# Performance work log

Hardware: AMD Instinct MI355X
Metric: run time of the kernel (lower is better)

The kernel has to match this reference:

```python
import jax, jax.numpy as jnp
import numpy as np

B, T, C, H = 4, 2048, 1024, 16
NEG = -1e9  # masked-fill value (finite to keep grads clean)


def setup_inputs() -> dict:
    key = jax.random.key(0)
    ks = jax.random.split(key, 5)
    s = 1.0 / np.sqrt(C)  # keep logits O(1) like trained linear layers
    return {
        "x": jax.random.normal(ks[0], (B, T, C), dtype=jnp.float32),
        "wq": jax.random.normal(ks[1], (C, C), dtype=jnp.float32) * s,
        "bq": jnp.zeros((C,), dtype=jnp.float32),
        "wk": jax.random.normal(ks[2], (C, C), dtype=jnp.float32) * s,
        "bk": jnp.zeros((C,), dtype=jnp.float32),
        "wv": jax.random.normal(ks[3], (C, C), dtype=jnp.float32) * s,
        "bv": jnp.zeros((C,), dtype=jnp.float32),
        "wo": jax.random.normal(ks[4], (C, C), dtype=jnp.float32) * s,
        "bo": jnp.zeros((C,), dtype=jnp.float32),
    }


def _split_heads(y):
    # [B,T,C] -> [B,H,T,hd]
    b, t, c = y.shape
    return y.reshape(b, t, H, c // H).transpose(0, 2, 1, 3)


def reference(x, wq, bq, wk, bk, wv, bv, wo, bo):
    b, t, c = x.shape
    scale = (c // H) ** (-0.5)
    q = _split_heads(x @ wq.T + bq)  # [B,H,T,hd]
    k = _split_heads(x @ wk.T + bk)
    v = _split_heads(x @ wv.T + bv)
    att = jnp.einsum("bhqd,bhkd->bhqk", q, k) * scale  # [B,H,T,T]
    causal = jnp.tril(jnp.ones((t, t), dtype=bool))
    att = jnp.where(causal[None, None], att, NEG)
    att = jax.nn.softmax(att, axis=-1)  # dropout is identity in eval mode
    y = jnp.einsum("bhqk,bhkd->bhqd", att, v)
    y = y.transpose(0, 2, 1, 3).reshape(b, t, c)
    return y @ wo.T + bo
```

## Files before the change

### kernel.cpp

```cpp
#include <hip/hip_runtime.h>


#define B_ 4
#define T_ 2048
#define C_ 1024
#define H_ 16
#define M_ 8192

typedef unsigned short u16;
typedef __bf16 bf16x8 __attribute__((ext_vector_type(8)));
typedef float f32x4 __attribute__((ext_vector_type(4)));

static __device__ __forceinline__ u16 f2bf(float f) {
  unsigned int u = __float_as_uint(f);
  u += 0x7fffu + ((u >> 16) & 1u);
  return (u16)(u >> 16);
}

static __device__ __forceinline__ void async16(const void* g, void* l) {
  __builtin_amdgcn_global_load_lds(
      (const __attribute__((address_space(1))) unsigned int*)g,
      (__attribute__((address_space(3))) unsigned int*)l, 16, 0, 0);
}

#if __has_builtin(__builtin_amdgcn_exp2f)
#define EXP2F(x) __builtin_amdgcn_exp2f(x)
#else
#define EXP2F(x) exp2f(x)
#endif

static __device__ __forceinline__ f32x4 mfma32(bf16x8 a, bf16x8 b, f32x4 c) {
  return __builtin_amdgcn_mfma_f32_16x16x32_bf16(a, b, c, 0, 0, 0);
}

static __device__ __forceinline__ unsigned int cvtpk(float lo, float hi) {
  unsigned int r;
  asm("v_cvt_pk_bf16_f32 %0, %1, %2" : "=v"(r) : "v"(lo), "v"(hi));
  return r;
}

#define FENCE() asm volatile("" ::: "memory")

__global__ __launch_bounds__(256) void cvt_all(const float* __restrict__ x,
                                               const float* __restrict__ w0,
                                               const float* __restrict__ w1,
                                               const float* __restrict__ w2,
                                               const float* __restrict__ w3,
                                               u16* __restrict__ xb,
                                               u16* __restrict__ wb,
                                               float s0) {
  const int NX = M_ * C_ / 4, NW = C_ * C_ / 4;
  int i = blockIdx.x * 256 + threadIdx.x;
  const float* src;
  u16* dst;
  int idx;
  float s = 1.f;
  if (i < NX) {
    src = x; dst = xb; idx = i;
  } else {
    int j = i - NX;
    int w = j / NW;
    idx = j - w * NW;
    src = (w == 0) ? w0 : (w == 1) ? w1 : (w == 2) ? w2 : w3;
    dst = wb + (size_t)w * C_ * C_;
    if (w == 0) s = s0;
  }
  float4 f = ((const float4*)src)[idx];
  ushort4 o;
  o.x = f2bf(f.x * s); o.y = f2bf(f.y * s); o.z = f2bf(f.z * s); o.w = f2bf(f.w * s);
  ((ushort4*)dst)[idx] = o;
}

__global__ __launch_bounds__(512, 1) void gemm_qkv(const u16* __restrict__ A,
                                                   const u16* __restrict__ W,
                                                   const float* __restrict__ bq,
                                                   const float* __restrict__ bk,
                                                   const float* __restrict__ bv,
                                                   float qscale,
                                                   u16* __restrict__ outqk,
                                                   u16* __restrict__ vtb) {
  __shared__ __align__(16) union {
    u16 buf[3][24576];
    u16 Cu[256 * 136];
    u16 Ct[128 * 272];
  } sm;
  const int tid = threadIdx.x, lane = tid & 63, wave = tid >> 6;
  const int quad = lane >> 4, l16 = lane & 15;
  const int wm = wave >> 1, wn = wave & 1;
  const int bid = blockIdx.x;
  const int xcd = bid & 7, idx = bid >> 3;
  const int cq = idx >> 2;
  const int row0 = (xcd * 4 + (idx & 3)) * 256;
  const int sel = cq >> 3, colw = cq & 7;
  const int col0 = colw * 128;
  const u16* Bt = W + (size_t)sel * C_ * C_;
  const float* bias = sel == 0 ? bq : (sel == 1 ? bk : bv);
  const float bscale = sel == 0 ? qscale : 1.f;

  const u16* aptr[4];
  const u16* bptr[2];
#pragma unroll
  for (int it = 0; it < 4; it++) {
    int c = it * 512 + tid, r = c >> 3, g = (c & 7) ^ (r & 7);
    aptr[it] = A + (size_t)(row0 + r) * C_ + g * 8;
  }
#pragma unroll
  for (int it = 0; it < 2; it++) {
    int c = it * 512 + tid, r = c >> 3, g = (c & 7) ^ (r & 7);
    bptr[it] = Bt + (size_t)(col0 + r) * C_ + g * 8;
  }

  auto STAGE = [&](int t, int pp) {
    const int k0 = t * 64;
    u16* lA = sm.buf[pp];
    u16* lB = sm.buf[pp] + 16384;
#pragma unroll
    for (int it = 0; it < 4; it++)
      async16(aptr[it] + k0, lA + (size_t)(it * 512 + wave * 64) * 8);
#pragma unroll
    for (int it = 0; it < 2; it++)
      async16(bptr[it] + k0, lB + (size_t)(it * 512 + wave * 64) * 8);
  };

  f32x4 zero = {0.f, 0.f, 0.f, 0.f};
  f32x4 acc[4][4];
#pragma unroll
  for (int i = 0; i < 4; i++)
#pragma unroll
    for (int j = 0; j < 4; j++) acc[i][j] = zero;

  STAGE(0, 0);
  STAGE(1, 1);

  int p = 0, p2 = 2;
#pragma unroll 1
  for (int u = 0; u < 16; ++u) {
    FENCE();
    __builtin_amdgcn_s_barrier();
    FENCE();
    if (u < 14) STAGE(u + 2, p2);
    if (u < 14) {
      asm volatile("s_waitcnt vmcnt(12)" ::: "memory");
    } else if (u < 15) {
      asm volatile("s_waitcnt vmcnt(6)" ::: "memory");
    } else {
      asm volatile("s_waitcnt vmcnt(0)" ::: "memory");
    }
    FENCE();
    __builtin_amdgcn_s_barrier();
    FENCE();

    const u16* As = sm.buf[p];
    const u16* Bs = sm.buf[p] + 16384;
    bf16x8 bfr[4][2];
#pragma unroll
    for (int j = 0; j < 4; j++) {
      int rn = wn * 64 + 16 * j + l16;
#pragma unroll
      for (int kk = 0; kk < 2; kk++)
        bfr[j][kk] =
            *(const bf16x8*)(Bs + rn * 64 + (((kk * 4 + quad) ^ (rn & 7)) * 8));
    }
    {
      bf16x8 a2[2][2];
#pragma unroll
      for (int i = 0; i < 2; i++) {
        int rm = wm * 64 + 16 * i + l16;
#pragma unroll
        for (int kk = 0; kk < 2; kk++)
          a2[i][kk] =
              *(const bf16x8*)(As + rm * 64 + (((kk * 4 + quad) ^ (rm & 7)) * 8));
      }
      __builtin_amdgcn_s_setprio(1);
#pragma unroll
      for (int i = 0; i < 2; i++)
#pragma unroll
        for (int j = 0; j < 4; j++) {
          acc[i][j] = mfma32(a2[i][0], bfr[j][0], acc[i][j]);
          acc[i][j] = mfma32(a2[i][1], bfr[j][1], acc[i][j]);
        }
      __builtin_amdgcn_s_setprio(0);
    }
    FENCE();
    __builtin_amdgcn_s_barrier();
    FENCE();
    {
      bf16x8 a2[2][2];
#pragma unroll
      for (int i = 0; i < 2; i++) {
        int rm = wm * 64 + 16 * (i + 2) + l16;
#pragma unroll
        for (int kk = 0; kk < 2; kk++)
          a2[i][kk] =
              *(const bf16x8*)(As + rm * 64 + (((kk * 4 + quad) ^ (rm & 7)) * 8));
      }
      __builtin_amdgcn_s_setprio(1);
#pragma unroll
      for (int i = 0; i < 2; i++)
#pragma unroll
        for (int j = 0; j < 4; j++) {
          acc[i + 2][j] = mfma32(a2[i][0], bfr[j][0], acc[i + 2][j]);
          acc[i + 2][j] = mfma32(a2[i][1], bfr[j][1], acc[i + 2][j]);
        }
      __builtin_amdgcn_s_setprio(0);
    }
    asm volatile("s_waitcnt lgkmcnt(0)" ::: "memory");
    p = (p == 2) ? 0 : p + 1;
    p2 = (p2 == 2) ? 0 : p2 + 1;
  }
  __syncthreads();

  float bj[4];
#pragma unroll
  for (int j = 0; j < 4; j++) bj[j] = bias[col0 + wn * 64 + 16 * j + l16] * bscale;

  if (sel == 2) {
#pragma unroll
    for (int i = 0; i < 4; i++)
#pragma unroll
      for (int j = 0; j < 4; j++) {
        int lc = wn * 64 + 16 * j + l16;
        int rt = wm * 64 + 16 * i + quad * 4;
        union { u16 s[4]; uint2 u; } w;
#pragma unroll
        for (int r = 0; r < 4; r++) w.s[r] = f2bf(acc[i][j][r] + bj[j]);
        *(uint2*)(sm.Ct + (size_t)lc * 272 + rt) = w.u;
      }
    __syncthreads();
    const int bb = row0 >> 11, t0 = row0 & 2047;
#pragma unroll
    for (int c2 = 0; c2 < 8; c2++) {
      int c = c2 * 512 + tid;
      int nr = c >> 5, ch = c & 31;
      bf16x8 v = *(const bf16x8*)(sm.Ct + (size_t)nr * 272 + ch * 8);
      int gn = col0 + nr, d = gn & 63, hh = gn >> 6;
      *(bf16x8*)(vtb + ((size_t)((bb * 16 + hh) * 64 + d)) * T_ + t0 + ch * 8) = v;
    }
  } else {
#pragma unroll
    for (int i = 0; i < 4; i++)
#pragma unroll
      for (int j = 0; j < 4; j++) {
        int lc = wn * 64 + 16 * j + l16;
        int rt = wm * 64 + 16 * i + quad * 4;
#pragma unroll
        for (int r = 0; r < 4; r++)
          sm.Cu[(size_t)(rt + r) * 136 + lc] = f2bf(acc[i][j][r] + bj[j]);
      }
    __syncthreads();
    u16* dst = outqk + (size_t)sel * M_ * C_;
#pragma unroll
    for (int c2 = 0; c2 < 8; c2++) {
      int c = c2 * 512 + tid;
      int rw = c >> 4, ch = c & 15;
      bf16x8 v = *(const bf16x8*)(sm.Cu + (size_t)rw * 136 + ch * 8);
      *(bf16x8*)(dst + (size_t)(row0 + rw) * C_ + col0 + ch * 8) = v;
    }
  }
}

__global__ __launch_bounds__(512, 1) void gemm_o(const u16* __restrict__ A,
                                                 const u16* __restrict__ Bt,
                                                 const float* __restrict__ bias,
                                                 float* __restrict__ outf) {
  __shared__ __align__(16) union {
    u16 buf[3][24576];
    float Cf[256 * 132];
  } sm;
  const int tid = threadIdx.x, lane = tid & 63, wave = tid >> 6;
  const int quad = lane >> 4, l16 = lane & 15;
  const int wm = wave >> 1, wn = wave & 1;
  const int bid = blockIdx.x;
  const int xcd = bid & 7, idx = bid >> 3;
  const int row0 = (xcd * 4 + (idx & 3)) * 256;
  const int col0 = (idx >> 2) * 128;

  const u16* aptr[4];
  const u16* bptr[2];
#pragma unroll
  for (int it = 0; it < 4; it++) {
    int c = it * 512 + tid, r = c >> 3, g = (c & 7) ^ (r & 7);
    aptr[it] = A + (size_t)(row0 + r) * C_ + g * 8;
  }
#pragma unroll
  for (int it = 0; it < 2; it++) {
    int c = it * 512 + tid, r = c >> 3, g = (c & 7) ^ (r & 7);
    bptr[it] = Bt + (size_t)(col0 + r) * C_ + g * 8;
  }

  auto STAGE = [&](int t, int pp) {
    const int k0 = t * 64;
    u16* lA = sm.buf[pp];
    u16* lB = sm.buf[pp] + 16384;
#pragma unroll
    for (int it = 0; it < 4; it++)
      async16(aptr[it] + k0, lA + (size_t)(it * 512 + wave * 64) * 8);
#pragma unroll
    for (int it = 0; it < 2; it++)
      async16(bptr[it] + k0, lB + (size_t)(it * 512 + wave * 64) * 8);
  };

  f32x4 zero = {0.f, 0.f, 0.f, 0.f};
  f32x4 acc[4][4];
#pragma unroll
  for (int i = 0; i < 4; i++)
#pragma unroll
    for (int j = 0; j < 4; j++) acc[i][j] = zero;

  STAGE(0, 0);
  STAGE(1, 1);

  int p = 0, p2 = 2;
#pragma unroll 1
  for (int u = 0; u < 16; ++u) {
    FENCE();
    __builtin_amdgcn_s_barrier();
    FENCE();
    if (u < 14) STAGE(u + 2, p2);
    if (u < 14) {
      asm volatile("s_waitcnt vmcnt(12)" ::: "memory");
    } else if (u < 15) {
      asm volatile("s_waitcnt vmcnt(6)" ::: "memory");
    } else {
      asm volatile("s_waitcnt vmcnt(0)" ::: "memory");
    }
    FENCE();
    __builtin_amdgcn_s_barrier();
    FENCE();

    const u16* As = sm.buf[p];
    const u16* Bs = sm.buf[p] + 16384;
    bf16x8 bfr[4][2];
#pragma unroll
    for (int j = 0; j < 4; j++) {
      int rn = wn * 64 + 16 * j + l16;
#pragma unroll
      for (int kk = 0; kk < 2; kk++)
        bfr[j][kk] =
            *(const bf16x8*)(Bs + rn * 64 + (((kk * 4 + quad) ^ (rn & 7)) * 8));
    }
    {
      bf16x8 a2[2][2];
#pragma unroll
      for (int i = 0; i < 2; i++) {
        int rm = wm * 64 + 16 * i + l16;
#pragma unroll
        for (int kk = 0; kk < 2; kk++)
          a2[i][kk] =
              *(const bf16x8*)(As + rm * 64 + (((kk * 4 + quad) ^ (rm & 7)) * 8));
      }
      __builtin_amdgcn_s_setprio(1);
#pragma unroll
      for (int i = 0; i < 2; i++)
#pragma unroll
        for (int j = 0; j < 4; j++) {
          acc[i][j] = mfma32(a2[i][0], bfr[j][0], acc[i][j]);
          acc[i][j] = mfma32(a2[i][1], bfr[j][1], acc[i][j]);
        }
      __builtin_amdgcn_s_setprio(0);
    }
    FENCE();
    __builtin_amdgcn_s_barrier();
    FENCE();
    {
      bf16x8 a2[2][2];
#pragma unroll
      for (int i = 0; i < 2; i++) {
        int rm = wm * 64 + 16 * (i + 2) + l16;
#pragma unroll
        for (int kk = 0; kk < 2; kk++)
          a2[i][kk] =
              *(const bf16x8*)(As + rm * 64 + (((kk * 4 + quad) ^ (rm & 7)) * 8));
      }
      __builtin_amdgcn_s_setprio(1);
#pragma unroll
      for (int i = 0; i < 2; i++)
#pragma unroll
        for (int j = 0; j < 4; j++) {
          acc[i + 2][j] = mfma32(a2[i][0], bfr[j][0], acc[i + 2][j]);
          acc[i + 2][j] = mfma32(a2[i][1], bfr[j][1], acc[i + 2][j]);
        }
      __builtin_amdgcn_s_setprio(0);
    }
    asm volatile("s_waitcnt lgkmcnt(0)" ::: "memory");
    p = (p == 2) ? 0 : p + 1;
    p2 = (p2 == 2) ? 0 : p2 + 1;
  }
  __syncthreads();

  float bj[4];
#pragma unroll
  for (int j = 0; j < 4; j++) bj[j] = bias[col0 + wn * 64 + 16 * j + l16];

#pragma unroll
  for (int i = 0; i < 4; i++)
#pragma unroll
    for (int j = 0; j < 4; j++) {
      int lc = wn * 64 + 16 * j + l16;
      int rt = wm * 64 + 16 * i + quad * 4;
#pragma unroll
      for (int r = 0; r < 4; r++)
        sm.Cf[(size_t)(rt + r) * 132 + lc] = acc[i][j][r] + bj[j];
    }
  __syncthreads();
#pragma unroll
  for (int c2 = 0; c2 < 16; c2++) {
    int c = c2 * 512 + tid;
    int rw = c >> 5, c4 = c & 31;
    float4 v = *(const float4*)(sm.Cf + (size_t)rw * 132 + c4 * 4);
    *(float4*)(outf + (size_t)(row0 + rw) * C_ + col0 + c4 * 4) = v;
  }
}

__global__ __launch_bounds__(256) void attn(const u16* __restrict__ q,
                                            const u16* __restrict__ k,
                                            const u16* __restrict__ vt,
                                            u16* __restrict__ y) {
  __shared__ __align__(16) u16 Ksm[128 * 64];
  __shared__ __align__(16) u16 Vsm[2][64 * 64];
  const int tid = threadIdx.x, lane = tid & 63, wave = tid >> 6;
  const int quad = lane >> 4, l16 = lane & 15;
  static const int qperm[16] = {15, 14, 11, 10, 12, 13, 8, 9, 3, 2, 7, 6, 0, 1, 4, 5};
  const int bh = blockIdx.x;
  const int qt = qperm[blockIdx.y];
  const int b = bh >> 4, h = bh & 15;

  const int S0 = ((lane & 15) + ((lane >> 4) & 1) * 32) * 4;
  const int S1 = S0 + 64;
  const bool hi32 = (lane & 32) != 0;

  bf16x8 qf[2][2];
#pragma unroll
  for (int m = 0; m < 2; m++) {
    const u16* qp =
        q + (size_t)(b * T_ + qt * 128 + wave * 32 + m * 16 + l16) * C_ + h * 64;
#pragma unroll
    for (int ks = 0; ks < 2; ks++)
      qf[m][ks] = *(const bf16x8*)(qp + ks * 32 + quad * 8);
  }

  f32x4 zero = {0.f, 0.f, 0.f, 0.f};
  f32x4 o[2][4];
  float lps[2] = {0.f, 0.f};
#pragma unroll
  for (int m = 0; m < 2; m++)
#pragma unroll
    for (int dt = 0; dt < 4; dt++) o[m][dt] = zero;

  const u16* kp[4];
  const u16* vp[4];
#pragma unroll
  for (int i = 0; i < 4; i++) {
    int c = i * 256 + tid;
    int r = c >> 3, lc = (c & 7) ^ (r & 7);
    kp[i] = k + (size_t)(b * T_ + r) * C_ + h * 64 + lc * 8;
  }
#pragma unroll
  for (int s = 0; s < 2; s++)
#pragma unroll
    for (int i = 0; i < 2; i++) {
      int c = i * 256 + tid;
      int r = c >> 3, lc = (c & 7) ^ (r & 7);
      vp[s * 2 + i] = vt + (size_t)(bh * 64 + r) * T_ + 64 * s + lc * 8;
    }

  const int qrow = wave * 32 + l16;

#pragma unroll 1
  for (int jt = 0; jt <= qt; ++jt) {
#pragma unroll
    for (int i = 0; i < 4; i++) {
      async16(kp[i], Ksm + (size_t)(i * 256 + wave * 64) * 8);
      kp[i] += (size_t)128 * C_;
    }
#pragma unroll
    for (int s = 0; s < 2; s++)
#pragma unroll
      for (int i = 0; i < 2; i++) {
        async16(vp[s * 2 + i], Vsm[s] + (size_t)(i * 256 + wave * 64) * 8);
        vp[s * 2 + i] += 128;
      }
    __syncthreads();

    const bool diag = (jt == qt);
#pragma unroll
    for (int hh = 0; hh < 2; ++hh) {
      if (diag && (2 * wave + 2 - 4 * hh) <= 0) continue;
      unsigned int pk[2][4][2];
#pragma unroll
      for (int n = 0; n < 4; ++n) {
        int rk = hh * 64 + n * 16 + l16;
        bf16x8 kf0 = *(const bf16x8*)(Ksm + rk * 64 + ((quad ^ (rk & 7)) * 8));
        bf16x8 kf1 = *(const bf16x8*)(Ksm + rk * 64 + (((4 + quad) ^ (rk & 7)) * 8));
#pragma unroll
        for (int m = 0; m < 2; ++m) {
          int nlim = diag ? (2 * wave + m + 1 - 4 * hh) : 4;
          float e[4];
          if (n < nlim) {
            f32x4 s = mfma32(kf0, qf[m][0], zero);
            s = mfma32(kf1, qf[m][1], s);
#pragma unroll
            for (int r = 0; r < 4; r++) e[r] = EXP2F(s[r]);
            if (diag) {
              int rmax = qrow + m * 16 - hh * 64 - n * 16 - quad * 4;
#pragma unroll
              for (int r = 0; r < 4; r++)
                if (r > rmax) e[r] = 0.f;
            }
            lps[m] += (e[0] + e[1]) + (e[2] + e[3]);
          } else {
#pragma unroll
            for (int r = 0; r < 4; r++) e[r] = 0.f;
          }
          pk[m][n][0] = cvtpk(e[0], e[1]);
          pk[m][n][1] = cvtpk(e[2], e[3]);
        }
      }
      bf16x8 pa[2][2];
#pragma unroll
      for (int m = 0; m < 2; ++m)
#pragma unroll
        for (int ks = 0; ks < 2; ++ks) {
          union { unsigned int u[4]; bf16x8 v; } uu;
#pragma unroll
          for (int c = 0; c < 2; ++c) {
            int x = (int)pk[m][2 * ks][c];
            int yv = (int)pk[m][2 * ks + 1][c];
            int bx0 = __builtin_amdgcn_ds_bpermute(S0, x);
            int by0 = __builtin_amdgcn_ds_bpermute(S0, yv);
            int bx1 = __builtin_amdgcn_ds_bpermute(S1, x);
            int by1 = __builtin_amdgcn_ds_bpermute(S1, yv);
            uu.u[c] = (unsigned int)(hi32 ? by0 : bx0);
            uu.u[2 + c] = (unsigned int)(hi32 ? by1 : bx1);
          }
          pa[m][ks] = uu.v;
        }
#pragma unroll
      for (int dt = 0; dt < 4; ++dt) {
        int rv = dt * 16 + l16;
        bf16x8 vf0 = *(const bf16x8*)(Vsm[hh] + rv * 64 + ((quad ^ (rv & 7)) * 8));
        bf16x8 vf1 = *(const bf16x8*)(Vsm[hh] + rv * 64 + (((4 + quad) ^ (rv & 7)) * 8));
#pragma unroll
        for (int m = 0; m < 2; m++) {
          o[m][dt] = mfma32(pa[m][0], vf0, o[m][dt]);
          o[m][dt] = mfma32(pa[m][1], vf1, o[m][dt]);
        }
      }
    }
    __syncthreads();
  }

  float linv[2];
#pragma unroll
  for (int m = 0; m < 2; m++) {
    float v = lps[m];
    v += __shfl_xor(v, 16);
    v += __shfl_xor(v, 32);
    linv[m] = 1.f / v;
  }

#pragma unroll
  for (int m = 0; m < 2; m++)
#pragma unroll
    for (int r = 0; r < 4; r++) {
      float il = __shfl(linv[m], quad * 4 + r);
      int grow = b * T_ + qt * 128 + wave * 32 + m * 16 + quad * 4 + r;
#pragma unroll
      for (int dt = 0; dt < 4; dt++)
        y[(size_t)grow * C_ + h * 64 + dt * 16 + l16] = f2bf(o[m][dt][r] * il);
    }
}

extern "C" void kernel_launch(void* const* d_in, const int* in_sizes, int n_in,
                              void* d_out, int out_size, void* d_ws, size_t ws_size,
                              hipStream_t stream) {
  const float* x  = (const float*)d_in[0];
  const float* wq = (const float*)d_in[1];
  const float* bq = (const float*)d_in[2];
  const float* wk = (const float*)d_in[3];
  const float* bk = (const float*)d_in[4];
  const float* wv = (const float*)d_in[5];
  const float* bv = (const float*)d_in[6];
  const float* wo = (const float*)d_in[7];
  const float* bo = (const float*)d_in[8];
  float* out = (float*)d_out;

  const float QSCALE = 0.125f * 1.4426950408889634f;

  u16* xb  = (u16*)d_ws;
  u16* wqb = xb  + (size_t)M_ * C_;
  u16* wob = wqb + 3 * (size_t)C_ * C_;
  u16* qb  = wob + (size_t)C_ * C_;
  u16* kb  = qb  + (size_t)M_ * C_;
  u16* vtb = kb  + (size_t)M_ * C_;
  u16* yb  = xb;

  const int NCVT = (M_ * C_ + 4 * C_ * C_) / 4 / 256;
  cvt_all<<<NCVT, 256, 0, stream>>>(x, wq, wk, wv, wo, xb, wqb, QSCALE);

  gemm_qkv<<<768, 512, 0, stream>>>(xb, wqb, bq, bk, bv, QSCALE, qb, vtb);

  attn<<<dim3(B_ * H_, 16), 256, 0, stream>>>(qb, kb, vtb, yb);

  gemm_o<<<256, 512, 0, stream>>>(yb, wob, bo, out);
}
```

Baseline: 251.5 us.

## Enlarge QKV GEMM tile to 256x256 with double-buffered LDS pipeline

Each QKV projection block now computes a 256x256 output tile instead of 256x128, and the grid shrinks from 768 to 384 blocks. Waves are arranged 2x4, and each wave holds 8x4 accumulators. The three-stage LDS ring is replaced by two buffers, with the next stage issued after the compute and its barrier. The aim is to raise arithmetic intensity and cut redundant A-tile loads. In exchange, register pressure rises, there is less latency hiding from the shallower pipeline, and 384 blocks may fill the 256 CUs unevenly.

Measured after the change: 255.0 us. No clear change (+1.4%).

```diff
diff --git a/kernel.cpp b/kernel.cpp
--- a/kernel.cpp
+++ b/kernel.cpp
@@ -80,33 +80,29 @@
                                                    u16* __restrict__ outqk,
                                                    u16* __restrict__ vtb) {
   __shared__ __align__(16) union {
-    u16 buf[3][24576];
-    u16 Cu[256 * 136];
-    u16 Ct[128 * 272];
+    u16 buf[2][32768];
+    u16 Cu[256 * 264];
+    u16 Ct[256 * 272];
   } sm;
   const int tid = threadIdx.x, lane = tid & 63, wave = tid >> 6;
   const int quad = lane >> 4, l16 = lane & 15;
-  const int wm = wave >> 1, wn = wave & 1;
+  const int wm = wave >> 2, wn = wave & 3;
   const int bid = blockIdx.x;
-  const int xcd = bid & 7, idx = bid >> 3;
-  const int cq = idx >> 2;
-  const int row0 = (xcd * 4 + (idx & 3)) * 256;
-  const int sel = cq >> 3, colw = cq & 7;
-  const int col0 = colw * 128;
+  const int xcd = bid & 7, lid = bid >> 3;
+  const int cq = lid >> 2, rloc = lid & 3;
+  const int row0 = (xcd * 4 + rloc) * 256;
+  const int sel = cq >> 2, colw = cq & 3;
+  const int col0 = colw * 256;
   const u16* Bt = W + (size_t)sel * C_ * C_;
   const float* bias = sel == 0 ? bq : (sel == 1 ? bk : bv);
   const float bscale = sel == 0 ? qscale : 1.f;
 
   const u16* aptr[4];
-  const u16* bptr[2];
+  const u16* bptr[4];
 #pragma unroll
   for (int it = 0; it < 4; it++) {
     int c = it * 512 + tid, r = c >> 3, g = (c & 7) ^ (r & 7);
     aptr[it] = A + (size_t)(row0 + r) * C_ + g * 8;
-  }
-#pragma unroll
-  for (int it = 0; it < 2; it++) {
-    int c = it * 512 + tid, r = c >> 3, g = (c & 7) ^ (r & 7);
     bptr[it] = Bt + (size_t)(col0 + r) * C_ + g * 8;
   }
 
@@ -118,31 +114,25 @@
     for (int it = 0; it < 4; it++)
       async16(aptr[it] + k0, lA + (size_t)(it * 512 + wave * 64) * 8);
 #pragma unroll
-    for (int it = 0; it < 2; it++)
+    for (int it = 0; it < 4; it++)
       async16(bptr[it] + k0, lB + (size_t)(it * 512 + wave * 64) * 8);
   };
 
   f32x4 zero = {0.f, 0.f, 0.f, 0.f};
-  f32x4 acc[4][4];
-#pragma unroll
-  for (int i = 0; i < 4; i++)
+  f32x4 acc[8][4];
+#pragma unroll
+  for (int i = 0; i < 8; i++)
 #pragma unroll
     for (int j = 0; j < 4; j++) acc[i][j] = zero;
 
   STAGE(0, 0);
   STAGE(1, 1);
 
-  int p = 0, p2 = 2;
 #pragma unroll 1
   for (int u = 0; u < 16; ++u) {
-    FENCE();
-    __builtin_amdgcn_s_barrier();
-    FENCE();
-    if (u < 14) STAGE(u + 2, p2);
-    if (u < 14) {
-      asm volatile("s_waitcnt vmcnt(12)" ::: "memory");
-    } else if (u < 15) {
-      asm volatile("s_waitcnt vmcnt(6)" ::: "memory");
+    const int cur = u & 1;
+    if (u < 15) {
+      asm volatile("s_waitcnt vmcnt(8)" ::: "memory");
     } else {
       asm volatile("s_waitcnt vmcnt(0)" ::: "memory");
     }
@@ -150,65 +140,40 @@
     __builtin_amdgcn_s_barrier();
     FENCE();
 
-    const u16* As = sm.buf[p];
-    const u16* Bs = sm.buf[p] + 16384;
-    bf16x8 bfr[4][2];
-#pragma unroll
-    for (int j = 0; j < 4; j++) {
-      int rn = wn * 64 + 16 * j + l16;
-#pragma unroll
-      for (int kk = 0; kk < 2; kk++)
-        bfr[j][kk] =
-            *(const bf16x8*)(Bs + rn * 64 + (((kk * 4 + quad) ^ (rn & 7)) * 8));
-    }
-    {
-      bf16x8 a2[2][2];
-#pragma unroll
-      for (int i = 0; i < 2; i++) {
-        int rm = wm * 64 + 16 * i + l16;
-#pragma unroll
-        for (int kk = 0; kk < 2; kk++)
-          a2[i][kk] =
-              *(const bf16x8*)(As + rm * 64 + (((kk * 4 + quad) ^ (rm & 7)) * 8));
+    const u16* As = sm.buf[cur];
+    const u16* Bs = sm.buf[cur] + 16384;
+#pragma unroll
+    for (int kk = 0; kk < 2; kk++) {
+      bf16x8 bv[4], av[8];
+#pragma unroll
+      for (int j = 0; j < 4; j++) {
+        int rn = wn * 64 + 16 * j + l16;
+        bv[j] = *(const bf16x8*)(Bs + rn * 64 + (((kk * 4 + quad) ^ (rn & 7)) * 8));
+      }
+#pragma unroll
+      for (int i = 0; i < 8; i++) {
+        int rm = wm * 128 + 16 * i + l16;
+        av[i] = *(const bf16x8*)(As + rm * 64 + (((kk * 4 + quad) ^ (rm & 7)) * 8));
       }
       __builtin_amdgcn_s_setprio(1);
 #pragma unroll
-      for (int i = 0; i < 2; i++)
-#pragma unroll
-        for (int j = 0; j < 4; j++) {
-          acc[i][j] = mfma32(a2[i][0], bfr[j][0], acc[i][j]);
-          acc[i][j] = mfma32(a2[i][1], bfr[j][1], acc[i][j]);
-        }
+      for (int i = 0; i < 8; i++)
+#pragma unroll
+        for (int j = 0; j < 4; j++)
+          acc[i][j] = mfma32(av[i], bv[j], acc[i][j]);
       __builtin_amdgcn_s_setprio(0);
-    }
+      if (kk == 0) {
+        FENCE();
+        __builtin_amdgcn_s_barrier();
+        FENCE();
+      }
+    }
+    asm volatile("s_waitcnt lgkmcnt(0)" ::: "memory");
     FENCE();
     __builtin_amdgcn_s_barrier();
     FENCE();
-    {
-      bf16x8 a2[2][2];
-#pragma unroll
-      for (int i = 0; i < 2; i++) {
-        int rm = wm * 64 + 16 * (i + 2) + l16;
-#pragma unroll
-        for (int kk = 0; kk < 2; kk++)
-          a2[i][kk] =
-              *(const bf16x8*)(As + rm * 64 + (((kk * 4 + quad) ^ (rm & 7)) * 8));
-      }
-      __builtin_amdgcn_s_setprio(1);
-#pragma unroll
-      for (int i = 0; i < 2; i++)
-#pragma unroll
-        for (int j = 0; j < 4; j++) {
-          acc[i + 2][j] = mfma32(a2[i][0], bfr[j][0], acc[i + 2][j]);
-          acc[i + 2][j] = mfma32(a2[i][1], bfr[j][1], acc[i + 2][j]);
-        }
-      __builtin_amdgcn_s_setprio(0);
-    }
-    asm volatile("s_waitcnt lgkmcnt(0)" ::: "memory");
-    p = (p == 2) ? 0 : p + 1;
-    p2 = (p2 == 2) ? 0 : p2 + 1;
-  }
-  __syncthreads();
+    if (u + 2 < 16) STAGE(u + 2, cur);
+  }
 
   float bj[4];
 #pragma unroll
@@ -216,11 +181,11 @@
 
   if (sel == 2) {
 #pragma unroll
-    for (int i = 0; i < 4; i++)
+    for (int i = 0; i < 8; i++)
 #pragma unroll
       for (int j = 0; j < 4; j++) {
         int lc = wn * 64 + 16 * j + l16;
-        int rt = wm * 64 + 16 * i + quad * 4;
+        int rt = wm * 128 + 16 * i + quad * 4;
         union { u16 s[4]; uint2 u; } w;
 #pragma unroll
         for (int r = 0; r < 4; r++) w.s[r] = f2bf(acc[i][j][r] + bj[j]);
@@ -229,7 +194,7 @@
     __syncthreads();
     const int bb = row0 >> 11, t0 = row0 & 2047;
 #pragma unroll
-    for (int c2 = 0; c2 < 8; c2++) {
+    for (int c2 = 0; c2 < 16; c2++) {
       int c = c2 * 512 + tid;
       int nr = c >> 5, ch = c & 31;
       bf16x8 v = *(const bf16x8*)(sm.Ct + (size_t)nr * 272 + ch * 8);
@@ -238,22 +203,22 @@
     }
   } else {
 #pragma unroll
-    for (int i = 0; i < 4; i++)
+    for (int i = 0; i < 8; i++)
 #pragma unroll
       for (int j = 0; j < 4; j++) {
         int lc = wn * 64 + 16 * j + l16;
-        int rt = wm * 64 + 16 * i + quad * 4;
+        int rt = wm * 128 + 16 * i + quad * 4;
 #pragma unroll
         for (int r = 0; r < 4; r++)
-          sm.Cu[(size_t)(rt + r) * 136 + lc] = f2bf(acc[i][j][r] + bj[j]);
+          sm.Cu[(size_t)(rt + r) * 264 + lc] = f2bf(acc[i][j][r] + bj[j]);
       }
     __syncthreads();
     u16* dst = outqk + (size_t)sel * M_ * C_;
 #pragma unroll
-    for (int c2 = 0; c2 < 8; c2++) {
+    for (int c2 = 0; c2 < 16; c2++) {
       int c = c2 * 512 + tid;
-      int rw = c >> 4, ch = c & 15;
-      bf16x8 v = *(const bf16x8*)(sm.Cu + (size_t)rw * 136 + ch * 8);
+      int rw = c >> 5, ch = c & 31;
+      bf16x8 v = *(const bf16x8*)(sm.Cu + (size_t)rw * 264 + ch * 8);
       *(bf16x8*)(dst + (size_t)(row0 + rw) * C_ + col0 + ch * 8) = v;
     }
   }
@@ -598,7 +563,7 @@
   const int NCVT = (M_ * C_ + 4 * C_ * C_) / 4 / 256;
   cvt_all<<<NCVT, 256, 0, stream>>>(x, wq, wk, wv, wo, xb, wqb, QSCALE);
 
-  gemm_qkv<<<768, 512, 0, stream>>>(xb, wqb, bq, bk, bv, QSCALE, qb, vtb);
+  gemm_qkv<<<384, 512, 0, stream>>>(xb, wqb, bq, bk, bv, QSCALE, qb, vtb);
 
   attn<<<dim3(B_ * H_, 16), 256, 0, stream>>>(qb, kb, vtb, yb);
 
```

## Interleave async global-to-LDS loads across four MFMA sub-phases per k-tile

Applied to the files above, without the earlier changes.

Restructures the main loop of the QKV and output-projection GEMMs. The async global-to-LDS staging of the next tile is now spread across four compute sub-phases split by k-half and row-half, instead of one bulk issue at the top of each iteration. The two barriers per iteration become four smaller phases, each reading LDS fragments, issuing one or two async copies, then running its MFMAs. The aim is to spread memory issue across the compute and shrink the stall at the tile boundary, at the cost of more barriers and lgkmcnt waits per k-tile.

Result: slower. 263.2 us (+4.7%).

```diff
diff --git a/kernel.cpp b/kernel.cpp
--- a/kernel.cpp
+++ b/kernel.cpp
@@ -40,6 +40,7 @@
 }
 
 #define FENCE() asm volatile("" ::: "memory")
+#define LGKM0() asm volatile("s_waitcnt lgkmcnt(0)" ::: "memory")
 
 __global__ __launch_bounds__(256) void cvt_all(const float* __restrict__ x,
                                                const float* __restrict__ w0,
@@ -110,16 +111,12 @@
     bptr[it] = Bt + (size_t)(col0 + r) * C_ + g * 8;
   }
 
-  auto STAGE = [&](int t, int pp) {
-    const int k0 = t * 64;
-    u16* lA = sm.buf[pp];
-    u16* lB = sm.buf[pp] + 16384;
-#pragma unroll
-    for (int it = 0; it < 4; it++)
-      async16(aptr[it] + k0, lA + (size_t)(it * 512 + wave * 64) * 8);
-#pragma unroll
-    for (int it = 0; it < 2; it++)
-      async16(bptr[it] + k0, lB + (size_t)(it * 512 + wave * 64) * 8);
+  auto SA = [&](int t, int pp, int it) {
+    async16(aptr[it] + t * 64, sm.buf[pp] + (size_t)(it * 512 + wave * 64) * 8);
+  };
+  auto SB = [&](int t, int pp, int it) {
+    async16(bptr[it] + t * 64,
+            sm.buf[pp] + 16384 + (size_t)(it * 512 + wave * 64) * 8);
   };
 
   f32x4 zero = {0.f, 0.f, 0.f, 0.f};
@@ -129,84 +126,113 @@
 #pragma unroll
     for (int j = 0; j < 4; j++) acc[i][j] = zero;
 
-  STAGE(0, 0);
-  STAGE(1, 1);
-
-  int p = 0, p2 = 2;
+#pragma unroll
+  for (int it = 0; it < 4; it++) SA(0, 0, it);
+  SB(0, 0, 0); SB(0, 0, 1);
+#pragma unroll
+  for (int it = 0; it < 4; it++) SA(1, 1, it);
+  SB(1, 1, 0); SB(1, 1, 1);
+  asm volatile("s_waitcnt vmcnt(6)" ::: "memory");
+  FENCE();
+  __builtin_amdgcn_s_barrier();
+  FENCE();
+
 #pragma unroll 1
-  for (int u = 0; u < 16; ++u) {
-    FENCE();
-    __builtin_amdgcn_s_barrier();
-    FENCE();
-    if (u < 14) STAGE(u + 2, p2);
-    if (u < 14) {
-      asm volatile("s_waitcnt vmcnt(12)" ::: "memory");
-    } else if (u < 15) {
-      asm volatile("s_waitcnt vmcnt(6)" ::: "memory");
-    } else {
-      asm volatile("s_waitcnt vmcnt(0)" ::: "memory");
-    }
-    FENCE();
-    __builtin_amdgcn_s_barrier();
-    FENCE();
-
-    const u16* As = sm.buf[p];
-    const u16* Bs = sm.buf[p] + 16384;
-    bf16x8 bfr[4][2];
-#pragma unroll
-    for (int j = 0; j < 4; j++) {
-      int rn = wn * 64 + 16 * j + l16;
-#pragma unroll
-      for (int kk = 0; kk < 2; kk++)
-        bfr[j][kk] =
-            *(const bf16x8*)(Bs + rn * 64 + (((kk * 4 + quad) ^ (rn & 7)) * 8));
-    }
-    {
-      bf16x8 a2[2][2];
-#pragma unroll
-      for (int i = 0; i < 2; i++) {
-        int rm = wm * 64 + 16 * i + l16;
-#pragma unroll
-        for (int kk = 0; kk < 2; kk++)
-          a2[i][kk] =
-              *(const bf16x8*)(As + rm * 64 + (((kk * 4 + quad) ^ (rm & 7)) * 8));
-      }
-      __builtin_amdgcn_s_setprio(1);
-#pragma unroll
-      for (int i = 0; i < 2; i++)
-#pragma unroll
-        for (int j = 0; j < 4; j++) {
-          acc[i][j] = mfma32(a2[i][0], bfr[j][0], acc[i][j]);
-          acc[i][j] = mfma32(a2[i][1], bfr[j][1], acc[i][j]);
-        }
-      __builtin_amdgcn_s_setprio(0);
-    }
-    FENCE();
-    __builtin_amdgcn_s_barrier();
-    FENCE();
-    {
-      bf16x8 a2[2][2];
-#pragma unroll
-      for (int i = 0; i < 2; i++) {
-        int rm = wm * 64 + 16 * (i + 2) + l16;
-#pragma unroll
-        for (int kk = 0; kk < 2; kk++)
-          a2[i][kk] =
-              *(const bf16x8*)(As + rm * 64 + (((kk * 4 + quad) ^ (rm & 7)) * 8));
-      }
-      __builtin_amdgcn_s_setprio(1);
-#pragma unroll
-      for (int i = 0; i < 2; i++)
-#pragma unroll
-        for (int j = 0; j < 4; j++) {
-          acc[i + 2][j] = mfma32(a2[i][0], bfr[j][0], acc[i + 2][j]);
-          acc[i + 2][j] = mfma32(a2[i][1], bfr[j][1], acc[i + 2][j]);
-        }
-      __builtin_amdgcn_s_setprio(0);
-    }
-    asm volatile("s_waitcnt lgkmcnt(0)" ::: "memory");
-    p = (p == 2) ? 0 : p + 1;
-    p2 = (p2 == 2) ? 0 : p2 + 1;
+  for (int t = 0; t < 16; ++t) {
+    const int cur = t % 3, dst = (t + 2) % 3;
+    const bool st = (t < 14);
+    const u16* As = sm.buf[cur];
+    const u16* Bs = sm.buf[cur] + 16384;
+
+    bf16x8 av0, av1, bv0[4];
+    {
+      int rm0 = wm * 64 + l16, rm1 = wm * 64 + 16 + l16;
+      av0 = *(const bf16x8*)(As + rm0 * 64 + ((quad ^ (rm0 & 7)) * 8));
+      av1 = *(const bf16x8*)(As + rm1 * 64 + ((quad ^ (rm1 & 7)) * 8));
+#pragma unroll
+      for (int j = 0; j < 4; j++) {
+        int rn = wn * 64 + 16 * j + l16;
+        bv0[j] = *(const bf16x8*)(Bs + rn * 64 + ((quad ^ (rn & 7)) * 8));
+      }
+      if (st) { SA(t + 2, dst, 0); SA(t + 2, dst, 1); }
+      LGKM0();
+      FENCE();
+      __builtin_amdgcn_s_setprio(1);
+#pragma unroll
+      for (int j = 0; j < 4; j++) {
+        acc[0][j] = mfma32(av0, bv0[j], acc[0][j]);
+        acc[1][j] = mfma32(av1, bv0[j], acc[1][j]);
+      }
+      __builtin_amdgcn_s_setprio(0);
+      FENCE();
+      __builtin_amdgcn_s_barrier();
+      FENCE();
+    }
+    {
+      int rm2 = wm * 64 + 32 + l16, rm3 = wm * 64 + 48 + l16;
+      bf16x8 av2 = *(const bf16x8*)(As + rm2 * 64 + ((quad ^ (rm2 & 7)) * 8));
+      bf16x8 av3 = *(const bf16x8*)(As + rm3 * 64 + ((quad ^ (rm3 & 7)) * 8));
+      if (st) { SA(t + 2, dst, 2); SA(t + 2, dst, 3); }
+      LGKM0();
+      FENCE();
+      __builtin_amdgcn_s_setprio(1);
+#pragma unroll
+      for (int j = 0; j < 4; j++) {
+        acc[2][j] = mfma32(av2, bv0[j], acc[2][j]);
+        acc[3][j] = mfma32(av3, bv0[j], acc[3][j]);
+      }
+      __builtin_amdgcn_s_setprio(0);
+      FENCE();
+      __builtin_amdgcn_s_barrier();
+      FENCE();
+    }
+    bf16x8 bv1[4];
+    {
+      int rm0 = wm * 64 + l16, rm1 = wm * 64 + 16 + l16;
+      bf16x8 av0b = *(const bf16x8*)(As + rm0 * 64 + (((4 + quad) ^ (rm0 & 7)) * 8));
+      bf16x8 av1b = *(const bf16x8*)(As + rm1 * 64 + (((4 + quad) ^ (rm1 & 7)) * 8));
+#pragma unroll
+      for (int j = 0; j < 4; j++) {
+        int rn = wn * 64 + 16 * j + l16;
+        bv1[j] = *(const bf16x8*)(Bs + rn * 64 + (((4 + quad) ^ (rn & 7)) * 8));
+      }
+      if (st) SB(t + 2, dst, 0);
+      LGKM0();
+      FENCE();
+      __builtin_amdgcn_s_setprio(1);
+#pragma unroll
+      for (int j = 0; j < 4; j++) {
+        acc[0][j] = mfma32(av0b, bv1[j], acc[0][j]);
+        acc[1][j] = mfma32(av1b, bv1[j], acc[1][j]);
+      }
+      __builtin_amdgcn_s_setprio(0);
+      FENCE();
+      __builtin_amdgcn_s_barrier();
+      FENCE();
+    }
+    {
+      int rm2 = wm * 64 + 32 + l16, rm3 = wm * 64 + 48 + l16;
+      bf16x8 av2b = *(const bf16x8*)(As + rm2 * 64 + (((4 + quad) ^ (rm2 & 7)) * 8));
+      bf16x8 av3b = *(const bf16x8*)(As + rm3 * 64 + (((4 + quad) ^ (rm3 & 7)) * 8));
+      if (st) SB(t + 2, dst, 1);
+      LGKM0();
+      FENCE();
+      __builtin_amdgcn_s_setprio(1);
+#pragma unroll
+      for (int j = 0; j < 4; j++) {
+        acc[2][j] = mfma32(av2b, bv1[j], acc[2][j]);
+        acc[3][j] = mfma32(av3b, bv1[j], acc[3][j]);
+      }
+      __builtin_amdgcn_s_setprio(0);
+      if (t <= 13) {
+        asm volatile("s_waitcnt vmcnt(6)" ::: "memory");
+      } else if (t == 14) {
+        asm volatile("s_waitcnt vmcnt(0)" ::: "memory");
+      }
+      FENCE();
+      __builtin_amdgcn_s_barrier();
+      FENCE();
+    }
   }
   __syncthreads();
 
@@ -248,13 +274,13 @@
           sm.Cu[(size_t)(rt + r) * 136 + lc] = f2bf(acc[i][j][r] + bj[j]);
       }
     __syncthreads();
-    u16* dst = outqk + (size_t)sel * M_ * C_;
+    u16* dst2 = outqk + (size_t)sel * M_ * C_;
 #pragma unroll
     for (int c2 = 0; c2 < 8; c2++) {
       int c = c2 * 512 + tid;
       int rw = c >> 4, ch = c & 15;
       bf16x8 v = *(const bf16x8*)(sm.Cu + (size_t)rw * 136 + ch * 8);
-      *(bf16x8*)(dst + (size_t)(row0 + rw) * C_ + col0 + ch * 8) = v;
+      *(bf16x8*)(dst2 + (size_t)(row0 + rw) * C_ + col0 + ch * 8) = v;
     }
   }
 }
@@ -288,16 +314,12 @@
     bptr[it] = Bt + (size_t)(col0 + r) * C_ + g * 8;
   }
 
-  auto STAGE = [&](int t, int pp) {
-    const int k0 = t * 64;
-    u16* lA = sm.buf[pp];
-    u16* lB = sm.buf[pp] + 16384;
-#pragma unroll
-    for (int it = 0; it < 4; it++)
-      async16(aptr[it] + k0, lA + (size_t)(it * 512 + wave * 64) * 8);
-#pragma unroll
-    for (int it = 0; it < 2; it++)
-      async16(bptr[it] + k0, lB + (size_t)(it * 512 + wave * 64) * 8);
+  auto SA = [&](int t, int pp, int it) {
+    async16(aptr[it] + t * 64, sm.buf[pp] + (size_t)(it * 512 + wave * 64) * 8);
+  };
+  auto SB = [&](int t, int pp, int it) {
+    async16(bptr[it] + t * 64,
+            sm.buf[pp] + 16384 + (size_t)(it * 512 + wave * 64) * 8);
   };
 
   f32x4 zero = {0.f, 0.f, 0.f, 0.f};
@@ -307,84 +329,113 @@
 #pragma unroll
     for (int j = 0; j < 4; j++) acc[i][j] = zero;
 
-  STAGE(0, 0);
-  STAGE(1, 1);
-
-  int p = 0, p2 = 2;
+#pragma unroll
+  for (int it = 0; it < 4; it++) SA(0, 0, it);
+  SB(0, 0, 0); SB(0, 0, 1);
+#pragma unroll
+  for (int it = 0; it < 4; it++) SA(1, 1, it);
+  SB(1, 1, 0); SB(1, 1, 1);
+  asm volatile("s_waitcnt vmcnt(6)" ::: "memory");
+  FENCE();
+  __builtin_amdgcn_s_barrier();
+  FENCE();
+
 #pragma unroll 1
-  for (int u = 0; u < 16; ++u) {
-    FENCE();
-    __builtin_amdgcn_s_barrier();
-    FENCE();
-    if (u < 14) STAGE(u + 2, p2);
-    if (u < 14) {
-      asm volatile("s_waitcnt vmcnt(12)" ::: "memory");
-    } else if (u < 15) {
-      asm volatile("s_waitcnt vmcnt(6)" ::: "memory");
-    } else {
-      asm volatile("s_waitcnt vmcnt(0)" ::: "memory");
-    }
-    FENCE();
-    __builtin_amdgcn_s_barrier();
-    FENCE();
-
-    const u16* As = sm.buf[p];
-    const u16* Bs = sm.buf[p] + 16384;
-    bf16x8 bfr[4][2];
-#pragma unroll
-    for (int j = 0; j < 4; j++) {
-      int rn = wn * 64 + 16 * j + l16;
-#pragma unroll
-      for (int kk = 0; kk < 2; kk++)
-        bfr[j][kk] =
-            *(const bf16x8*)(Bs + rn * 64 + (((kk * 4 + quad) ^ (rn & 7)) * 8));
-    }
-    {
-      bf16x8 a2[2][2];
-#pragma unroll
-      for (int i = 0; i < 2; i++) {
-        int rm = wm * 64 + 16 * i + l16;
-#pragma unroll
-        for (int kk = 0; kk < 2; kk++)
-          a2[i][kk] =
-              *(const bf16x8*)(As + rm * 64 + (((kk * 4 + quad) ^ (rm & 7)) * 8));
-      }
-      __builtin_amdgcn_s_setprio(1);
-#pragma unroll
-      for (int i = 0; i < 2; i++)
-#pragma unroll
-        for (int j = 0; j < 4; j++) {
-          acc[i][j] = mfma32(a2[i][0], bfr[j][0], acc[i][j]);
-          acc[i][j] = mfma32(a2[i][1], bfr[j][1], acc[i][j]);
-        }
-      __builtin_amdgcn_s_setprio(0);
-    }
-    FENCE();
-    __builtin_amdgcn_s_barrier();
-    FENCE();
-    {
-      bf16x8 a2[2][2];
-#pragma unroll
-      for (int i = 0; i < 2; i++) {
-        int rm = wm * 64 + 16 * (i + 2) + l16;
-#pragma unroll
-        for (int kk = 0; kk < 2; kk++)
-          a2[i][kk] =
-              *(const bf16x8*)(As + rm * 64 + (((kk * 4 + quad) ^ (rm & 7)) * 8));
-      }
-      __builtin_amdgcn_s_setprio(1);
-#pragma unroll
-      for (int i = 0; i < 2; i++)
-#pragma unroll
-        for (int j = 0; j < 4; j++) {
-          acc[i + 2][j] = mfma32(a2[i][0], bfr[j][0], acc[i + 2][j]);
-          acc[i + 2][j] = mfma32(a2[i][1], bfr[j][1], acc[i + 2][j]);
-        }
-      __builtin_amdgcn_s_setprio(0);
-    }
-    asm volatile("s_waitcnt lgkmcnt(0)" ::: "memory");
-    p = (p == 2) ? 0 : p + 1;
-    p2 = (p2 == 2) ? 0 : p2 + 1;
+  for (int t = 0; t < 16; ++t) {
+    const int cur = t % 3, dst = (t + 2) % 3;
+    const bool st = (t < 14);
+    const u16* As = sm.buf[cur];
+    const u16* Bs = sm.buf[cur] + 16384;
+
+    bf16x8 av0, av1, bv0[4];
+    {
+      int rm0 = wm * 64 + l16, rm1 = wm * 64 + 16 + l16;
+      av0 = *(const bf16x8*)(As + rm0 * 64 + ((quad ^ (rm0 & 7)) * 8));
+      av1 = *(const bf16x8*)(As + rm1 * 64 + ((quad ^ (rm1 & 7)) * 8));
+#pragma unroll
+      for (int j = 0; j < 4; j++) {
+        int rn = wn * 64 + 16 * j + l16;
+        bv0[j] = *(const bf16x8*)(Bs + rn * 64 + ((quad ^ (rn & 7)) * 8));
+      }
+      if (st) { SA(t + 2, dst, 0); SA(t + 2, dst, 1); }
+      LGKM0();
+      FENCE();
+      __builtin_amdgcn_s_setprio(1);
+#pragma unroll
+      for (int j = 0; j < 4; j++) {
+        acc[0][j] = mfma32(av0, bv0[j], acc[0][j]);
+        acc[1][j] = mfma32(av1, bv0[j], acc[1][j]);
+      }
+      __builtin_amdgcn_s_setprio(0);
+      FENCE();
+      __builtin_amdgcn_s_barrier();
+      FENCE();
+    }
+    {
+      int rm2 = wm * 64 + 32 + l16, rm3 = wm * 64 + 48 + l16;
+      bf16x8 av2 = *(const bf16x8*)(As + rm2 * 64 + ((quad ^ (rm2 & 7)) * 8));
+      bf16x8 av3 = *(const bf16x8*)(As + rm3 * 64 + ((quad ^ (rm3 & 7)) * 8));
+      if (st) { SA(t + 2, dst, 2); SA(t + 2, dst, 3); }
+      LGKM0();
+      FENCE();
+      __builtin_amdgcn_s_setprio(1);
+#pragma unroll
+      for (int j = 0; j < 4; j++) {
+        acc[2][j] = mfma32(av2, bv0[j], acc[2][j]);
+        acc[3][j] = mfma32(av3, bv0[j], acc[3][j]);
+      }
+      __builtin_amdgcn_s_setprio(0);
+      FENCE();
+      __builtin_amdgcn_s_barrier();
+      FENCE();
+    }
+    bf16x8 bv1[4];
+    {
+      int rm0 = wm * 64 + l16, rm1 = wm * 64 + 16 + l16;
+      bf16x8 av0b = *(const bf16x8*)(As + rm0 * 64 + (((4 + quad) ^ (rm0 & 7)) * 8));
+      bf16x8 av1b = *(const bf16x8*)(As + rm1 * 64 + (((4 + quad) ^ (rm1 & 7)) * 8));
+#pragma unroll
+      for (int j = 0; j < 4; j++) {
+        int rn = wn * 64 + 16 * j + l16;
+        bv1[j] = *(const bf16x8*)(Bs + rn * 64 + (((4 + quad) ^ (rn & 7)) * 8));
+      }
+      if (st) SB(t + 2, dst, 0);
+      LGKM0();
+      FENCE();
+      __builtin_amdgcn_s_setprio(1);
+#pragma unroll
+      for (int j = 0; j < 4; j++) {
+        acc[0][j] = mfma32(av0b, bv1[j], acc[0][j]);
+        acc[1][j] = mfma32(av1b, bv1[j], acc[1][j]);
+      }
+      __builtin_amdgcn_s_setprio(0);
+      FENCE();
+      __builtin_amdgcn_s_barrier();
+      FENCE();
+    }
+    {
+      int rm2 = wm * 64 + 32 + l16, rm3 = wm * 64 + 48 + l16;
+      bf16x8 av2b = *(const bf16x8*)(As + rm2 * 64 + (((4 + quad) ^ (rm2 & 7)) * 8));
+      bf16x8 av3b = *(const bf16x8*)(As + rm3 * 64 + (((4 + quad) ^ (rm3 & 7)) * 8));
+      if (st) SB(t + 2, dst, 1);
+      LGKM0();
+      FENCE();
+      __builtin_amdgcn_s_setprio(1);
+#pragma unroll
+      for (int j = 0; j < 4; j++) {
+        acc[2][j] = mfma32(av2b, bv1[j], acc[2][j]);
+        acc[3][j] = mfma32(av3b, bv1[j], acc[3][j]);
+      }
+      __builtin_amdgcn_s_setprio(0);
+      if (t <= 13) {
+        asm volatile("s_waitcnt vmcnt(6)" ::: "memory");
+      } else if (t == 14) {
+        asm volatile("s_waitcnt vmcnt(0)" ::: "memory");
+      }
+      FENCE();
+      __builtin_amdgcn_s_barrier();
+      FENCE();
+    }
   }
   __syncthreads();
 
```

## Double-buffer K/V tiles in attention to overlap loads with compute

Applied to the files above, without the earlier changes.

Allocates two LDS buffers each for the K and V tiles. At the top of each iteration the kernel issues the async global-to-LDS loads for the next KV tile into the spare buffer, then computes on the current one, and the trailing barrier is dropped. This hides global-load latency behind the MFMA and softmax work. In exchange LDS use per block doubles, to 64 KB, which can lower occupancy, and correctness relies on the barrier waiting for the outstanding async loads.

New measurement: 269.0 us. 7.0% more time.

```diff
diff --git a/kernel.cpp b/kernel.cpp
--- a/kernel.cpp
+++ b/kernel.cpp
@@ -416,8 +416,8 @@
                                             const u16* __restrict__ k,
                                             const u16* __restrict__ vt,
                                             u16* __restrict__ y) {
-  __shared__ __align__(16) u16 Ksm[128 * 64];
-  __shared__ __align__(16) u16 Vsm[2][64 * 64];
+  __shared__ __align__(16) u16 Ksm[2][128 * 64];
+  __shared__ __align__(16) u16 Vsm[2][2][64 * 64];
   const int tid = threadIdx.x, lane = tid & 63, wave = tid >> 6;
   const int quad = lane >> 4, l16 = lane & 15;
   static const int qperm[16] = {15, 14, 11, 10, 12, 13, 8, 9, 3, 2, 7, 6, 0, 1, 4, 5};
@@ -464,23 +464,28 @@
       vp[s * 2 + i] = vt + (size_t)(bh * 64 + r) * T_ + 64 * s + lc * 8;
     }
 
+  auto stageKV = [&](int jt, int ss) {
+    const size_t koff = (size_t)jt * 128 * C_;
+    const int voff = jt * 128;
+#pragma unroll
+    for (int i = 0; i < 4; i++)
+      async16(kp[i] + koff, Ksm[ss] + (size_t)(i * 256 + wave * 64) * 8);
+#pragma unroll
+    for (int s = 0; s < 2; s++)
+#pragma unroll
+      for (int i = 0; i < 2; i++)
+        async16(vp[s * 2 + i] + voff, Vsm[ss][s] + (size_t)(i * 256 + wave * 64) * 8);
+  };
+
   const int qrow = wave * 32 + l16;
+
+  stageKV(0, 0);
 
 #pragma unroll 1
   for (int jt = 0; jt <= qt; ++jt) {
-#pragma unroll
-    for (int i = 0; i < 4; i++) {
-      async16(kp[i], Ksm + (size_t)(i * 256 + wave * 64) * 8);
-      kp[i] += (size_t)128 * C_;
-    }
-#pragma unroll
-    for (int s = 0; s < 2; s++)
-#pragma unroll
-      for (int i = 0; i < 2; i++) {
-        async16(vp[s * 2 + i], Vsm[s] + (size_t)(i * 256 + wave * 64) * 8);
-        vp[s * 2 + i] += 128;
-      }
+    const int cs = jt & 1;
     __syncthreads();
+    if (jt < qt) stageKV(jt + 1, cs ^ 1);
 
     const bool diag = (jt == qt);
 #pragma unroll
@@ -490,8 +495,8 @@
 #pragma unroll
       for (int n = 0; n < 4; ++n) {
         int rk = hh * 64 + n * 16 + l16;
-        bf16x8 kf0 = *(const bf16x8*)(Ksm + rk * 64 + ((quad ^ (rk & 7)) * 8));
-        bf16x8 kf1 = *(const bf16x8*)(Ksm + rk * 64 + (((4 + quad) ^ (rk & 7)) * 8));
+        bf16x8 kf0 = *(const bf16x8*)(Ksm[cs] + rk * 64 + ((quad ^ (rk & 7)) * 8));
+        bf16x8 kf1 = *(const bf16x8*)(Ksm[cs] + rk * 64 + (((4 + quad) ^ (rk & 7)) * 8));
 #pragma unroll
         for (int m = 0; m < 2; ++m) {
           int nlim = diag ? (2 * wave + m + 1 - 4 * hh) : 4;
@@ -538,8 +543,9 @@
 #pragma unroll
       for (int dt = 0; dt < 4; ++dt) {
         int rv = dt * 16 + l16;
-        bf16x8 vf0 = *(const bf16x8*)(Vsm[hh] + rv * 64 + ((quad ^ (rv & 7)) * 8));
-        bf16x8 vf1 = *(const bf16x8*)(Vsm[hh] + rv * 64 + (((4 + quad) ^ (rv & 7)) * 8));
+        bf16x8 vf0 = *(const bf16x8*)(Vsm[cs][hh] + rv * 64 + ((quad ^ (rv & 7)) * 8));
+        bf16x8 vf1 =
+            *(const bf16x8*)(Vsm[cs][hh] + rv * 64 + (((4 + quad) ^ (rv & 7)) * 8));
 #pragma unroll
         for (int m = 0; m < 2; m++) {
           o[m][dt] = mfma32(pa[m][0], vf0, o[m][dt]);
@@ -547,7 +553,6 @@
         }
       }
     }
-    __syncthreads();
   }
 
   float linv[2];
```
